# Kernel optimization log

Measured on AMD Instinct MI355X. Metric: run time of the kernel, lower is better.

## Reference

```python
import jax, jax.numpy as jnp
import numpy as np

N = 100000   # nodes
E = 1_600_000  # edges (avg degree 16)
D = 64       # input_dim = hidden_dim = output_dim
EPS = 1e-5   # BatchNorm eps


def setup_inputs() -> dict:
    key = jax.random.key(0)
    ks = jax.random.split(key, 8)
    x = jax.random.normal(ks[0], (N, D), jnp.float32)
    edge_index = jax.random.randint(ks[1], (2, E), 0, N, jnp.int32)

    def lin_w(k, din, dout):
        s = 1.0 / np.sqrt(din)
        return jax.random.uniform(k, (din, dout), jnp.float32, -s, s)

    return {
        "x": x, "edge_index": edge_index,
        "W1": lin_w(ks[2], D, D), "b1": jnp.zeros((D,), jnp.float32),
        "g1": jnp.ones((D,), jnp.float32), "be1": jnp.zeros((D,), jnp.float32),
        "W2": lin_w(ks[3], D, D), "b2": jnp.zeros((D,), jnp.float32),
        "g2": jnp.ones((D,), jnp.float32), "be2": jnp.zeros((D,), jnp.float32),
        "W3": lin_w(ks[4], D, D), "b3": jnp.zeros((D,), jnp.float32),
        "g3": jnp.ones((D,), jnp.float32), "be3": jnp.zeros((D,), jnp.float32),
    }


def gcn_conv(x, src, dst, W, b):
    # GCNConv: out = D^{-1/2}(A+I)D^{-1/2} (x @ W) + b
    n = x.shape[0]
    loops = jnp.arange(n, dtype=src.dtype)
    s = jnp.concatenate([src, loops])  # add self-loops
    d = jnp.concatenate([dst, loops])
    deg = jax.ops.segment_sum(jnp.ones_like(s, jnp.float32), d, num_segments=n)
    dinv = jax.lax.rsqrt(jnp.maximum(deg, 1.0))  # deg >= 1 (self-loops)
    norm = dinv[s] * dinv[d]                     # [E+N]
    xw = x @ W                                   # [N, D]
    msgs = xw[s] * norm[:, None]                 # [E+N, D] gather
    return jax.ops.segment_sum(msgs, d, num_segments=n) + b  # scatter-add


def batch_norm(z, g, be):
    # training-mode BatchNorm1d: batch statistics, biased variance
    mu = jnp.mean(z, axis=0)
    var = jnp.mean(jnp.square(z - mu), axis=0)
    return (z - mu) * jax.lax.rsqrt(var + EPS) * g + be


def reference(x, edge_index, W1, b1, g1, be1, W2, b2, g2, be2, W3, b3, g3, be3):
    src, dst = edge_index[0], edge_index[1]
    z = jax.nn.relu(batch_norm(gcn_conv(x, src, dst, W1, b1), g1, be1))
    z = jax.nn.relu(batch_norm(gcn_conv(z, src, dst, W2, b2), g2, be2))
    z = batch_norm(gcn_conv(z, src, dst, W3, b3), g3, be3)
    # dropout (p=0.1) is identity in eval mode; normalize=False default
    return z
```

## Files before the change

kernel.cpp:

```cpp
#include <hip/hip_runtime.h>

typedef unsigned short ushort_t;
typedef unsigned int uint_t;
typedef float f32x4 __attribute__((ext_vector_type(4)));
typedef short bf16x8 __attribute__((ext_vector_type(8)));

#define NB_AGG 2048
#define BSHIFT 7
#define BROWS 128
#define BCAP 4096
#define NCHUNK 256
#define ZP 72

__device__ __forceinline__ float bf2f_lo(uint_t u) {
    union { uint_t i; float f; } v; v.i = u << 16; return v.f;
}
__device__ __forceinline__ float bf2f_hi(uint_t u) {
    union { uint_t i; float f; } v; v.i = u & 0xffff0000u; return v.f;
}
__device__ __forceinline__ ushort_t f2bf(float f) {
    union { float f; uint_t i; } v; v.f = f;
    uint_t u = v.i;
    uint_t r = (u + 0x7fffu + ((u >> 16) & 1u)) >> 16;
    return (ushort_t)r;
}

__global__ __launch_bounds__(256) void hist2_k(const int* __restrict__ dst,
                                               int* __restrict__ H, int E, int nb) {
    __shared__ int h[1024];
    int b = blockIdx.x, t = threadIdx.x;
    for (int i = t; i < nb; i += 256) h[i] = 0;
    __syncthreads();
    int per = (E + NCHUNK - 1) / NCHUNK;
    int lo = b * per, hi = min(E, lo + per);
    for (int e = lo + t; e < hi; e += 256)
        atomicAdd(&h[dst[e] >> BSHIFT], 1);
    __syncthreads();
    for (int i = t; i < nb; i += 256) H[(size_t)i * NCHUNK + b] = h[i];
}

__global__ __launch_bounds__(256) void scanA_k(const int* __restrict__ v,
                                               int* __restrict__ segsum, int total) {
    int base = blockIdx.x * 1024 + threadIdx.x;
    int s = 0;
#pragma unroll
    for (int i = 0; i < 4; ++i) {
        int idx = base + i * 256;
        if (idx < total) s += v[idx];
    }
    __shared__ int sh[256];
    sh[threadIdx.x] = s;
    __syncthreads();
    for (int off = 128; off > 0; off >>= 1) {
        if (threadIdx.x < off) sh[threadIdx.x] += sh[threadIdx.x + off];
        __syncthreads();
    }
    if (threadIdx.x == 0) segsum[blockIdx.x] = sh[0];
}

__global__ void scanB_k(int* segsum, int nseg) {
    __shared__ int sh[256];
    int t = threadIdx.x;
    int own = (t < nseg) ? segsum[t] : 0;
    sh[t] = own;
    __syncthreads();
    for (int off = 1; off < 256; off <<= 1) {
        int v = (t >= off) ? sh[t - off] : 0;
        __syncthreads();
        sh[t] += v;
        __syncthreads();
    }
    if (t < nseg) segsum[t] = sh[t] - own;
}

__global__ __launch_bounds__(256) void scanC2_k(int* __restrict__ H,
                                                const int* __restrict__ segsum,
                                                int total) {
    int t = threadIdx.x;
    int base = blockIdx.x * 1024 + t * 4;
    int c0 = 0, c1 = 0, c2 = 0, c3 = 0;
    if (base + 0 < total) c0 = H[base + 0];
    if (base + 1 < total) c1 = H[base + 1];
    if (base + 2 < total) c2 = H[base + 2];
    if (base + 3 < total) c3 = H[base + 3];
    int tsum = c0 + c1 + c2 + c3;
    __shared__ int sh[256];
    sh[t] = tsum;
    __syncthreads();
    for (int off = 1; off < 256; off <<= 1) {
        int v = (t >= off) ? sh[t - off] : 0;
        __syncthreads();
        sh[t] += v;
        __syncthreads();
    }
    int excl = segsum[blockIdx.x] + sh[t] - tsum;
    if (base + 0 < total) H[base + 0] = excl;
    if (base + 1 < total) H[base + 1] = excl + c0;
    if (base + 2 < total) H[base + 2] = excl + c0 + c1;
    if (base + 3 < total) H[base + 3] = excl + c0 + c1 + c2;
}

__global__ __launch_bounds__(256) void scat2_k(const int* __restrict__ src,
                                               const int* __restrict__ dst,
                                               const int* __restrict__ H,
                                               int* __restrict__ colA, int E, int nb) {
    __shared__ int cur[1024];
    int b = blockIdx.x, t = threadIdx.x;
    for (int i = t; i < nb; i += 256) cur[i] = H[(size_t)i * NCHUNK + b];
    __syncthreads();
    int per = (E + NCHUNK - 1) / NCHUNK;
    int lo = b * per, hi = min(E, lo + per);
    for (int e = lo + t; e < hi; e += 256) {
        int d = dst[e];
        int bk = d >> BSHIFT;
        int pos = atomicAdd(&cur[bk], 1);
        colA[pos] = (src[e] << BSHIFT) | (d & (BROWS - 1));
    }
}

__global__ __launch_bounds__(256) void build_k(int* __restrict__ colA,
                                               const int* __restrict__ H,
                                               float* __restrict__ dinv,
                                               int* __restrict__ rowp,
                                               int N, int E, int nb) {
    __shared__ int recs[BCAP];
    __shared__ int cnt[BROWS], pfx[BROWS], cur[BROWS];
    int b = blockIdx.x, t = threadIdx.x;
    int base = H[(size_t)b * NCHUNK];
    int next = (b + 1 < nb) ? H[(size_t)(b + 1) * NCHUNK] : E;
    int size = next - base;
    if (size > BCAP) size = BCAP;
    int row0 = b << BSHIFT;

    if (t < BROWS) { cnt[t] = 0; cur[t] = 0; }
    __syncthreads();

    for (int i = t; i < size; i += 256) {
        int r = colA[base + i];
        recs[i] = r;
        atomicAdd(&cnt[r & (BROWS - 1)], 1);
    }
    __syncthreads();

    if (t < BROWS) pfx[t] = cnt[t];
    __syncthreads();
    for (int off = 1; off < BROWS; off <<= 1) {
        int u = 0;
        if (t < BROWS && t >= off) u = pfx[t - off];
        __syncthreads();
        if (t < BROWS) pfx[t] += u;
        __syncthreads();
    }
    if (t < BROWS) {
        int row = row0 + t;
        if (row < N) {
            int ex = pfx[t] - cnt[t];
            rowp[row] = base + ex;
            dinv[row] = rsqrtf((float)cnt[t] + 1.0f);
            if (row == N - 1) rowp[N] = base + pfx[t];
        }
    }
    __syncthreads();

    for (int i = t; i < size; i += 256) {
        int r = recs[i];
        int l = r & (BROWS - 1);
        int pos = base + (pfx[l] - cnt[l]) + atomicAdd(&cur[l], 1);
        colA[pos] = r >> BSHIFT;
    }
}

__global__ __launch_bounds__(256) void wconv_k(const float* __restrict__ W1,
                                               const float* __restrict__ W2,
                                               const float* __restrict__ W3,
                                               ushort_t* __restrict__ Wb) {
    int t = blockIdx.x * 256 + threadIdx.x;
    if (t >= 3 * 4096) return;
    int l = t >> 12, i = t & 4095;
    int col = i >> 6, k = i & 63;
    const float* W = (l == 0) ? W1 : ((l == 1) ? W2 : W3);
    Wb[(size_t)l * 4096 + col * 64 + k] = f2bf(W[k * 64 + col]);
}

template <int MODE>
__global__ __launch_bounds__(256) void gemm_k(const float* __restrict__ Zf,
                                              const uint2* __restrict__ Zb,
                                              const ushort_t* __restrict__ Wb,
                                              const float* __restrict__ dinv,
                                              const float* __restrict__ cA,
                                              const float* __restrict__ cC,
                                              ushort_t* __restrict__ XW, int N) {
    __shared__ ushort_t WbT[64 * ZP];
    __shared__ ushort_t Zt[64 * ZP];
    __shared__ ushort_t Ot[4][16 * ZP];
    __shared__ float Al[64], Cl[64], Dl[64];
    int t = threadIdx.x;
    int row0 = blockIdx.x * 64;

    if (t < 64) {
        int r = row0 + t;
        Dl[t] = (r < N) ? dinv[r] : 0.0f;
        if (MODE) { Al[t] = cA[t]; Cl[t] = cC[t]; }
    }
    {
        const uint4* ws = (const uint4*)Wb;
#pragma unroll
        for (int i = 0; i < 2; ++i) {
            int cid = t * 2 + i;
            int col = cid >> 3, seg = cid & 7;
            *(uint4*)&WbT[col * ZP + seg * 8] = ws[cid];
        }
    }
    __syncthreads();

    {
        int r = t >> 2, cg = t & 3;
        int grow = row0 + r;
        bool gv = grow < N;
#pragma unroll
        for (int q = 0; q < 4; ++q) {
            float4 v;
            if (MODE) {
                uint2 p2 = {0, 0};
                if (gv) p2 = Zb[(size_t)grow * 16 + cg * 4 + q];
                v.x = bf2f_lo(p2.x); v.y = bf2f_hi(p2.x);
                v.z = bf2f_lo(p2.y); v.w = bf2f_hi(p2.y);
                int k = cg * 16 + q * 4;
                v.x = fmaxf(Al[k + 0] * v.x + Cl[k + 0], 0.0f);
                v.y = fmaxf(Al[k + 1] * v.y + Cl[k + 1], 0.0f);
                v.z = fmaxf(Al[k + 2] * v.z + Cl[k + 2], 0.0f);
                v.w = fmaxf(Al[k + 3] * v.w + Cl[k + 3], 0.0f);
            } else {
                if (gv) v = *(const float4*)(Zf + (size_t)grow * 64 + cg * 16 + q * 4);
                else { v.x = v.y = v.z = v.w = 0.0f; }
            }
            uint2 p;
            p.x = (uint_t)f2bf(v.x) | ((uint_t)f2bf(v.y) << 16);
            p.y = (uint_t)f2bf(v.z) | ((uint_t)f2bf(v.w) << 16);
            *(uint2*)&Zt[r * ZP + cg * 16 + q * 4] = p;
        }
    }
    __syncthreads();

    int wv = t >> 6, lane = t & 63;
    int mrow = lane & 15;
    int kgrp = lane >> 4;

    f32x4 acc0 = {0, 0, 0, 0}, acc1 = {0, 0, 0, 0};
    f32x4 acc2 = {0, 0, 0, 0}, acc3 = {0, 0, 0, 0};
#pragma unroll
    for (int ks = 0; ks < 2; ++ks) {
        bf16x8 a = *(bf16x8*)&Zt[(wv * 16 + mrow) * ZP + ks * 32 + kgrp * 8];
        bf16x8 b0 = *(bf16x8*)&WbT[(0 + mrow) * ZP + ks * 32 + kgrp * 8];
        bf16x8 b1 = *(bf16x8*)&WbT[(16 + mrow) * ZP + ks * 32 + kgrp * 8];
        bf16x8 b2 = *(bf16x8*)&WbT[(32 + mrow) * ZP + ks * 32 + kgrp * 8];
        bf16x8 b3 = *(bf16x8*)&WbT[(48 + mrow) * ZP + ks * 32 + kgrp * 8];
        acc0 = __builtin_amdgcn_mfma_f32_16x16x32_bf16(a, b0, acc0, 0, 0, 0);
        acc1 = __builtin_amdgcn_mfma_f32_16x16x32_bf16(a, b1, acc1, 0, 0, 0);
        acc2 = __builtin_amdgcn_mfma_f32_16x16x32_bf16(a, b2, acc2, 0, 0, 0);
        acc3 = __builtin_amdgcn_mfma_f32_16x16x32_bf16(a, b3, acc3, 0, 0, 0);
    }

#pragma unroll
    for (int r = 0; r < 4; ++r) {
        int orow = kgrp * 4 + r;
        float dn = Dl[wv * 16 + orow];
        Ot[wv][orow * ZP + 0 + mrow]  = f2bf(acc0[r] * dn);
        Ot[wv][orow * ZP + 16 + mrow] = f2bf(acc1[r] * dn);
        Ot[wv][orow * ZP + 32 + mrow] = f2bf(acc2[r] * dn);
        Ot[wv][orow * ZP + 48 + mrow] = f2bf(acc3[r] * dn);
    }
#pragma unroll
    for (int i = 0; i < 2; ++i) {
        int cid = lane * 2 + i;
        int orow = cid >> 3, seg = cid & 7;
        int grow = row0 + wv * 16 + orow;
        if (grow < N)
            *(uint4*)(XW + (size_t)grow * 64 + seg * 8) =
                *(uint4*)&Ot[wv][orow * ZP + seg * 8];
    }
}

__global__ __launch_bounds__(256) void agg_k(const ushort_t* __restrict__ y,
                                             const int* __restrict__ row_ptr,
                                             const int* __restrict__ colA,
                                             const float* __restrict__ dinv,
                                             uint2* __restrict__ OUTB,
                                             float* __restrict__ pS,
                                             float* __restrict__ pQ, int N) {
    __shared__ float ssum[64], ssq[64];
    int t = threadIdx.x, lane = t & 63, wv = t >> 6;
    int rs = lane >> 5;
    int g = (lane >> 4) & 1;
    int c = lane & 15;
    if (t < 64) ssum[t] = 0.0f;
    else if (t < 128) ssq[t - 64] = 0.0f;
    __syncthreads();

    const uint2* y2 = (const uint2*)y;
    float ps0 = 0, ps1 = 0, ps2 = 0, ps3 = 0;
    float pq0 = 0, pq1 = 0, pq2 = 0, pq3 = 0;

    int npair = (N + 1) >> 1;
    for (int p = blockIdx.x * 4 + wv; p < npair; p += NB_AGG * 4) {
        int row = p * 2 + rs;
        bool rv = row < N;
        int rc = rv ? row : N - 1;
        int start = row_ptr[rc];
        int end = row_ptr[rc + 1];
        int len = rv ? (end - start) : 0;
        int ml = max(len, __shfl_xor(len, 32));

        float a0 = 0, a1 = 0, a2 = 0, a3 = 0;
        for (int off = 0; off < ml; off += 16) {
            int sA[8];
            uint_t mA[8];
#pragma unroll
            for (int u = 0; u < 8; ++u) {
                int slot = off + u * 2 + g;
                bool val = slot < len;
                int ec = val ? (start + slot) : 0;
                sA[u] = colA[ec];
                mA[u] = val ? 0xffffffffu : 0u;
            }
#pragma unroll
            for (int u = 0; u < 8; ++u) {
                uint2 v = y2[(size_t)sA[u] * 16 + c];
                v.x &= mA[u]; v.y &= mA[u];
                a0 += bf2f_lo(v.x);
                a1 += bf2f_hi(v.x);
                a2 += bf2f_lo(v.y);
                a3 += bf2f_hi(v.y);
            }
        }

        a0 += __shfl_xor(a0, 16);
        a1 += __shfl_xor(a1, 16);
        a2 += __shfl_xor(a2, 16);
        a3 += __shfl_xor(a3, 16);

        if (g == 0 && rv) {
            float dn = dinv[row];
            uint2 sv = y2[(size_t)row * 16 + c];
            float v0 = dn * (a0 + bf2f_lo(sv.x));
            float v1 = dn * (a1 + bf2f_hi(sv.x));
            float v2 = dn * (a2 + bf2f_lo(sv.y));
            float v3 = dn * (a3 + bf2f_hi(sv.y));
            uint2 pk;
            pk.x = (uint_t)f2bf(v0) | ((uint_t)f2bf(v1) << 16);
            pk.y = (uint_t)f2bf(v2) | ((uint_t)f2bf(v3) << 16);
            OUTB[(size_t)row * 16 + c] = pk;
            ps0 += v0; ps1 += v1; ps2 += v2; ps3 += v3;
            pq0 += v0 * v0; pq1 += v1 * v1; pq2 += v2 * v2; pq3 += v3 * v3;
        }
    }

    if (g == 0) {
        atomicAdd(&ssum[c * 4 + 0], ps0); atomicAdd(&ssq[c * 4 + 0], pq0);
        atomicAdd(&ssum[c * 4 + 1], ps1); atomicAdd(&ssq[c * 4 + 1], pq1);
        atomicAdd(&ssum[c * 4 + 2], ps2); atomicAdd(&ssq[c * 4 + 2], pq2);
        atomicAdd(&ssum[c * 4 + 3], ps3); atomicAdd(&ssq[c * 4 + 3], pq3);
    }
    __syncthreads();
    if (t < 64) pS[(size_t)t * NB_AGG + blockIdx.x] = ssum[t];
    else if (t < 128) pQ[(size_t)(t - 64) * NB_AGG + blockIdx.x] = ssq[t - 64];
}

__global__ __launch_bounds__(256) void stats_k(const float* __restrict__ pS,
                                               const float* __restrict__ pQ,
                                               const float* __restrict__ g,
                                               const float* __restrict__ be,
                                               float* __restrict__ cA,
                                               float* __restrict__ cC, int N) {
    int c = blockIdx.x, t = threadIdx.x;
    float s = 0.0f, q = 0.0f;
    for (int i = t; i < NB_AGG; i += 256) {
        s += pS[(size_t)c * NB_AGG + i];
        q += pQ[(size_t)c * NB_AGG + i];
    }
    __shared__ float rs[256], rq[256];
    rs[t] = s; rq[t] = q;
    __syncthreads();
    for (int off = 128; off > 0; off >>= 1) {
        if (t < off) { rs[t] += rs[t + off]; rq[t] += rq[t + off]; }
        __syncthreads();
    }
    if (t == 0) {
        float mu = rs[0] / (float)N;
        float var = rq[0] / (float)N - mu * mu;
        var = fmaxf(var, 0.0f);
        float inv = rsqrtf(var + 1e-5f);
        float a = g[c] * inv;
        cA[c] = a;
        cC[c] = be[c] - mu * a;
    }
}

__global__ __launch_bounds__(256) void apply_k(const uint2* __restrict__ Zb,
                                               float* __restrict__ O,
                                               const float* __restrict__ cA,
                                               const float* __restrict__ cC,
                                               int N) {
    int total = N * 16;
    for (int i = blockIdx.x * 256 + threadIdx.x; i < total; i += gridDim.x * 256) {
        uint2 p = Zb[i];
        int c = (i & 15) * 4;
        float4 v;
        v.x = cA[c + 0] * bf2f_lo(p.x) + cC[c + 0];
        v.y = cA[c + 1] * bf2f_hi(p.x) + cC[c + 1];
        v.z = cA[c + 2] * bf2f_lo(p.y) + cC[c + 2];
        v.w = cA[c + 3] * bf2f_hi(p.y) + cC[c + 3];
        ((float4*)O)[i] = v;
    }
}

extern "C" void kernel_launch(void* const* d_in, const int* in_sizes, int n_in,
                              void* d_out, int out_size, void* d_ws, size_t ws_size,
                              hipStream_t stream) {
    const float* x   = (const float*)d_in[0];
    const int*   ei  = (const int*)d_in[1];
    const float* W1  = (const float*)d_in[2];
    const float* g1  = (const float*)d_in[4];
    const float* be1 = (const float*)d_in[5];
    const float* W2  = (const float*)d_in[6];
    const float* g2  = (const float*)d_in[8];
    const float* be2 = (const float*)d_in[9];
    const float* W3  = (const float*)d_in[10];
    const float* g3  = (const float*)d_in[12];
    const float* be3 = (const float*)d_in[13];

    int N = in_sizes[0] / 64;
    int E = in_sizes[1] / 2;
    const int* srcA = ei;
    const int* dstA = ei + E;
    int nb = (N + BROWS - 1) >> BSHIFT;
    int total = nb * NCHUNK;
    int nseg = (total + 1023) / 1024;

    char* w = (char*)d_ws;
    auto alloc = [&](size_t bytes) -> char* {
        char* p = w;
        w += (bytes + 255) & ~(size_t)255;
        return p;
    };
    ushort_t* xw    = (ushort_t*)alloc((size_t)N * 64 * 2);
    uint2*    zb    = (uint2*)alloc((size_t)N * 64 * 2);
    ushort_t* Wb    = (ushort_t*)alloc((size_t)3 * 4096 * 2);
    int*      rowp  = (int*)alloc(((size_t)N + 1) * 4);
    float*    dinv  = (float*)alloc((size_t)N * 4);
    int*      colA  = (int*)alloc((size_t)E * 4);
    int*      H     = (int*)alloc((size_t)total * 4);
    int*      segsum= (int*)alloc((size_t)nseg * 4);
    float*    pS    = (float*)alloc((size_t)64 * NB_AGG * 4);
    float*    pQ    = (float*)alloc((size_t)64 * NB_AGG * 4);
    float*    cA1 = (float*)alloc(256); float* cC1 = (float*)alloc(256);
    float*    cA2 = (float*)alloc(256); float* cC2 = (float*)alloc(256);
    float*    cA3 = (float*)alloc(256); float* cC3 = (float*)alloc(256);
    (void)ws_size; (void)n_in; (void)out_size;

    float* out = (float*)d_out;

    hist2_k<<<NCHUNK, 256, 0, stream>>>(dstA, H, E, nb);
    scanA_k<<<nseg, 256, 0, stream>>>(H, segsum, total);
    scanB_k<<<1, 256, 0, stream>>>(segsum, nseg);
    scanC2_k<<<nseg, 256, 0, stream>>>(H, segsum, total);
    scat2_k<<<NCHUNK, 256, 0, stream>>>(srcA, dstA, H, colA, E, nb);
    build_k<<<nb, 256, 0, stream>>>(colA, H, dinv, rowp, N, E, nb);
    wconv_k<<<48, 256, 0, stream>>>(W1, W2, W3, Wb);

    int gemmGrid = (N + 63) / 64;

    gemm_k<0><<<gemmGrid, 256, 0, stream>>>(x, nullptr, Wb, dinv, nullptr, nullptr, xw, N);
    agg_k<<<NB_AGG, 256, 0, stream>>>(xw, rowp, colA, dinv, zb, pS, pQ, N);
    stats_k<<<64, 256, 0, stream>>>(pS, pQ, g1, be1, cA1, cC1, N);

    gemm_k<1><<<gemmGrid, 256, 0, stream>>>(nullptr, zb, Wb + 4096, dinv, cA1, cC1, xw, N);
    agg_k<<<NB_AGG, 256, 0, stream>>>(xw, rowp, colA, dinv, zb, pS, pQ, N);
    stats_k<<<64, 256, 0, stream>>>(pS, pQ, g2, be2, cA2, cC2, N);

    gemm_k<1><<<gemmGrid, 256, 0, stream>>>(nullptr, zb, Wb + 8192, dinv, cA2, cC2, xw, N);
    agg_k<<<NB_AGG, 256, 0, stream>>>(xw, rowp, colA, dinv, zb, pS, pQ, N);
    stats_k<<<64, 256, 0, stream>>>(pS, pQ, g3, be3, cA3, cC3, N);

    apply_k<<<2048, 256, 0, stream>>>(zb, out, cA3, cC3, N);
}
```

Before: 236.2 us.

## Sort rows by degree for aggregation and fold BN stats into atomic replicas

Adds a counting sort of nodes by in-degree (histogram, scan, scatter) so that the aggregation kernel's two rows per wave have similar lengths, which cuts divergence and idle lanes. It also replaces the per-block partial-sum buffers and the 64-block stats reduction with global atomics into 32 replicated accumulators, read by a single-block stats kernel that also clears them. In exchange it adds three small preprocessing kernels and a memset, and the permuted row order scatters output writes and spreads row_ptr reads.

```diff
diff --git a/kernel.cpp b/kernel.cpp
--- a/kernel.cpp
+++ b/kernel.cpp
@@ -11,6 +11,7 @@
 #define BCAP 4096
 #define NCHUNK 256
 #define ZP 72
+#define NREP 32
 
 __device__ __forceinline__ float bf2f_lo(uint_t u) {
     union { uint_t i; float f; } v; v.i = u << 16; return v.f;
@@ -167,6 +168,58 @@
         int l = r & (BROWS - 1);
         int pos = base + (pfx[l] - cnt[l]) + atomicAdd(&cur[l], 1);
         colA[pos] = r >> BSHIFT;
+    }
+}
+
+__global__ __launch_bounds__(256) void dsA_k(const int* __restrict__ rowp,
+                                             int* __restrict__ DH, int N) {
+    __shared__ int h[64];
+    int b = blockIdx.x, t = threadIdx.x;
+    if (t < 64) h[t] = 0;
+    __syncthreads();
+    int per = (N + 63) / 64;
+    int lo = b * per, hi = min(N, lo + per);
+    for (int r = lo + t; r < hi; r += 256) {
+        int deg = rowp[r + 1] - rowp[r];
+        atomicAdd(&h[min(deg, 63)], 1);
+    }
+    __syncthreads();
+    if (t < 64) DH[t * 64 + b] = h[t];
+}
+
+__global__ void dscan_k(int* __restrict__ DH) {
+    __shared__ int sh[256];
+    int t = threadIdx.x;
+    int c[16];
+    int s = 0;
+#pragma unroll
+    for (int i = 0; i < 16; ++i) { c[i] = DH[t * 16 + i]; s += c[i]; }
+    sh[t] = s;
+    __syncthreads();
+    for (int off = 1; off < 256; off <<= 1) {
+        int v = (t >= off) ? sh[t - off] : 0;
+        __syncthreads();
+        sh[t] += v;
+        __syncthreads();
+    }
+    int run = sh[t] - s;
+#pragma unroll
+    for (int i = 0; i < 16; ++i) { DH[t * 16 + i] = run; run += c[i]; }
+}
+
+__global__ __launch_bounds__(256) void dsB_k(const int* __restrict__ rowp,
+                                             const int* __restrict__ DH,
+                                             int* __restrict__ perm, int N) {
+    __shared__ int cur[64];
+    int b = blockIdx.x, t = threadIdx.x;
+    if (t < 64) cur[t] = DH[t * 64 + b];
+    __syncthreads();
+    int per = (N + 63) / 64;
+    int lo = b * per, hi = min(N, lo + per);
+    for (int r = lo + t; r < hi; r += 256) {
+        int deg = rowp[r + 1] - rowp[r];
+        int pos = atomicAdd(&cur[min(deg, 63)], 1);
+        perm[pos] = r;
     }
 }
 
@@ -284,10 +337,10 @@
 __global__ __launch_bounds__(256) void agg_k(const ushort_t* __restrict__ y,
                                              const int* __restrict__ row_ptr,
                                              const int* __restrict__ colA,
+                                             const int* __restrict__ perm,
                                              const float* __restrict__ dinv,
                                              uint2* __restrict__ OUTB,
-                                             float* __restrict__ pS,
-                                             float* __restrict__ pQ, int N) {
+                                             float* __restrict__ gstat, int N) {
     __shared__ float ssum[64], ssq[64];
     int t = threadIdx.x, lane = t & 63, wv = t >> 6;
     int rs = lane >> 5;
@@ -303,11 +356,12 @@
 
     int npair = (N + 1) >> 1;
     for (int p = blockIdx.x * 4 + wv; p < npair; p += NB_AGG * 4) {
-        int row = p * 2 + rs;
-        bool rv = row < N;
-        int rc = rv ? row : N - 1;
-        int start = row_ptr[rc];
-        int end = row_ptr[rc + 1];
+        int idx = p * 2 + rs;
+        bool rv = idx < N;
+        int ic = rv ? idx : N - 1;
+        int row = perm[ic];
+        int start = row_ptr[row];
+        int end = row_ptr[row + 1];
         int len = rv ? (end - start) : 0;
         int ml = max(len, __shfl_xor(len, 32));
 
@@ -362,38 +416,31 @@
         atomicAdd(&ssum[c * 4 + 3], ps3); atomicAdd(&ssq[c * 4 + 3], pq3);
     }
     __syncthreads();
-    if (t < 64) pS[(size_t)t * NB_AGG + blockIdx.x] = ssum[t];
-    else if (t < 128) pQ[(size_t)(t - 64) * NB_AGG + blockIdx.x] = ssq[t - 64];
-}
-
-__global__ __launch_bounds__(256) void stats_k(const float* __restrict__ pS,
-                                               const float* __restrict__ pQ,
-                                               const float* __restrict__ g,
-                                               const float* __restrict__ be,
-                                               float* __restrict__ cA,
-                                               float* __restrict__ cC, int N) {
-    int c = blockIdx.x, t = threadIdx.x;
-    float s = 0.0f, q = 0.0f;
-    for (int i = t; i < NB_AGG; i += 256) {
-        s += pS[(size_t)c * NB_AGG + i];
-        q += pQ[(size_t)c * NB_AGG + i];
-    }
-    __shared__ float rs[256], rq[256];
-    rs[t] = s; rq[t] = q;
-    __syncthreads();
-    for (int off = 128; off > 0; off >>= 1) {
-        if (t < off) { rs[t] += rs[t + off]; rq[t] += rq[t + off]; }
-        __syncthreads();
-    }
-    if (t == 0) {
-        float mu = rs[0] / (float)N;
-        float var = rq[0] / (float)N - mu * mu;
-        var = fmaxf(var, 0.0f);
-        float inv = rsqrtf(var + 1e-5f);
-        float a = g[c] * inv;
-        cA[c] = a;
-        cC[c] = be[c] - mu * a;
-    }
+    float* gr = gstat + (size_t)(blockIdx.x & (NREP - 1)) * 128;
+    if (t < 64) atomicAdd(&gr[t], ssum[t]);
+    else if (t < 128) atomicAdd(&gr[t], ssq[t - 64]);
+}
+
+__global__ void stats2_k(float* __restrict__ gstat,
+                         const float* __restrict__ g,
+                         const float* __restrict__ be,
+                         float* __restrict__ cA,
+                         float* __restrict__ cC, int N) {
+    int t = threadIdx.x;
+    if (t < 64) {
+        float s = 0.0f, q = 0.0f;
+        for (int r = 0; r < NREP; ++r) {
+            s += gstat[r * 128 + t];
+            q += gstat[r * 128 + 64 + t];
+        }
+        float mu = s / (float)N;
+        float var = fmaxf(q / (float)N - mu * mu, 0.0f);
+        float a = g[t] * rsqrtf(var + 1e-5f);
+        cA[t] = a;
+        cC[t] = be[t] - mu * a;
+    }
+    __syncthreads();
+    for (int i = t; i < NREP * 128; i += 256) gstat[i] = 0.0f;
 }
 
 __global__ __launch_bounds__(256) void apply_k(const uint2* __restrict__ Zb,
@@ -449,10 +496,11 @@
     int*      rowp  = (int*)alloc(((size_t)N + 1) * 4);
     float*    dinv  = (float*)alloc((size_t)N * 4);
     int*      colA  = (int*)alloc((size_t)E * 4);
+    int*      perm  = (int*)alloc((size_t)N * 4);
     int*      H     = (int*)alloc((size_t)total * 4);
+    int*      DH    = (int*)alloc((size_t)4096 * 4);
     int*      segsum= (int*)alloc((size_t)nseg * 4);
-    float*    pS    = (float*)alloc((size_t)64 * NB_AGG * 4);
-    float*    pQ    = (float*)alloc((size_t)64 * NB_AGG * 4);
+    float*    gstat = (float*)alloc((size_t)NREP * 128 * 4);
     float*    cA1 = (float*)alloc(256); float* cC1 = (float*)alloc(256);
     float*    cA2 = (float*)alloc(256); float* cC2 = (float*)alloc(256);
     float*    cA3 = (float*)alloc(256); float* cC3 = (float*)alloc(256);
@@ -460,27 +508,31 @@
 
     float* out = (float*)d_out;
 
+    hipMemsetAsync(gstat, 0, (size_t)NREP * 128 * 4, stream);
     hist2_k<<<NCHUNK, 256, 0, stream>>>(dstA, H, E, nb);
     scanA_k<<<nseg, 256, 0, stream>>>(H, segsum, total);
     scanB_k<<<1, 256, 0, stream>>>(segsum, nseg);
     scanC2_k<<<nseg, 256, 0, stream>>>(H, segsum, total);
     scat2_k<<<NCHUNK, 256, 0, stream>>>(srcA, dstA, H, colA, E, nb);
     build_k<<<nb, 256, 0, stream>>>(colA, H, dinv, rowp, N, E, nb);
+    dsA_k<<<64, 256, 0, stream>>>(rowp, DH, N);
+    dscan_k<<<1, 256, 0, stream>>>(DH);
+    dsB_k<<<64, 256, 0, stream>>>(rowp, DH, perm, N);
     wconv_k<<<48, 256, 0, stream>>>(W1, W2, W3, Wb);
 
     int gemmGrid = (N + 63) / 64;
 
     gemm_k<0><<<gemmGrid, 256, 0, stream>>>(x, nullptr, Wb, dinv, nullptr, nullptr, xw, N);
-    agg_k<<<NB_AGG, 256, 0, stream>>>(xw, rowp, colA, dinv, zb, pS, pQ, N);
-    stats_k<<<64, 256, 0, stream>>>(pS, pQ, g1, be1, cA1, cC1, N);
+    agg_k<<<NB_AGG, 256, 0, stream>>>(xw, rowp, colA, perm, dinv, zb, gstat, N);
+    stats2_k<<<1, 256, 0, stream>>>(gstat, g1, be1, cA1, cC1, N);
 
     gemm_k<1><<<gemmGrid, 256, 0, stream>>>(nullptr, zb, Wb + 4096, dinv, cA1, cC1, xw, N);
-    agg_k<<<NB_AGG, 256, 0, stream>>>(xw, rowp, colA, dinv, zb, pS, pQ, N);
-    stats_k<<<64, 256, 0, stream>>>(pS, pQ, g2, be2, cA2, cC2, N);
+    agg_k<<<NB_AGG, 256, 0, stream>>>(xw, rowp, colA, perm, dinv, zb, gstat, N);
+    stats2_k<<<1, 256, 0, stream>>>(gstat, g2, be2, cA2, cC2, N);
 
     gemm_k<1><<<gemmGrid, 256, 0, stream>>>(nullptr, zb, Wb + 8192, dinv, cA2, cC2, xw, N);
-    agg_k<<<NB_AGG, 256, 0, stream>>>(xw, rowp, colA, dinv, zb, pS, pQ, N);
-    stats_k<<<64, 256, 0, stream>>>(pS, pQ, g3, be3, cA3, cC3, N);
+    agg_k<<<NB_AGG, 256, 0, stream>>>(xw, rowp, colA, perm, dinv, zb, gstat, N);
+    stats2_k<<<1, 256, 0, stream>>>(gstat, g3, be3, cA3, cC3, N);
 
     apply_k<<<2048, 256, 0, stream>>>(zb, out, cA3, cC3, N);
 }
```

Result: slower. 243.3 us (+3.0%).
